# Performance work log

Measured on AMD Instinct MI355X. Metric: run time of the kernel, lower is better.

Reference implementation:

```python
import jax, jax.numpy as jnp
import numpy as np

NUM_HEADS = 12
EMBED_DIM = 768
HEAD_DIM = EMBED_DIM // NUM_HEADS


def _rope_cos_sin():
    # Faithful to source: RoPE is applied with seq_dim=1 on [b,h,n,d] tensors,
    # so the "position" axis is actually the HEAD axis (length NUM_HEADS).
    inv_freq = 1.0 / (10000.0 ** (jnp.arange(0, HEAD_DIM, 2, dtype=jnp.float32) / HEAD_DIM))
    t = jnp.arange(NUM_HEADS, dtype=jnp.float32)
    freqs = t[:, None] * inv_freq[None, :]            # [H, D/2]
    emb = jnp.concatenate([freqs, freqs], axis=-1)     # [H, D]
    cos = jnp.cos(emb)[None, :, None, :]               # [1, H, 1, D] broadcasts over seq
    sin = jnp.sin(emb)[None, :, None, :]
    return cos, sin


def _apply_rope(x, cos, sin):
    # x: [B, H, N, D]
    x1, x2 = jnp.split(x, 2, axis=-1)
    x_rot = jnp.concatenate([-x2, x1], axis=-1)
    return x * cos + x_rot * sin


def setup_inputs() -> dict:
    key = jax.random.key(0)
    k1, k2, k3, k4, k5 = jax.random.split(key, 5)
    B, N, E = 8, 1024, EMBED_DIM
    s_in = 1.0 / np.sqrt(E)
    return {
        "x": jax.random.normal(k1, (B, N, E), dtype=jnp.float32),
        "w_qkv": jax.random.uniform(k2, (E, 3 * E), dtype=jnp.float32, minval=-s_in, maxval=s_in),
        "b_qkv": jax.random.uniform(k3, (3 * E,), dtype=jnp.float32, minval=-s_in, maxval=s_in),
        "w_proj": jax.random.uniform(k4, (E, E), dtype=jnp.float32, minval=-s_in, maxval=s_in),
        "b_proj": jax.random.uniform(k5, (E,), dtype=jnp.float32, minval=-s_in, maxval=s_in),
    }


def reference(x, w_qkv, b_qkv, w_proj, b_proj):
    B, N, E = x.shape
    H, D = NUM_HEADS, HEAD_DIM
    scale = D ** (-0.5)

    qkv = x @ w_qkv + b_qkv                                  # [B, N, 3E]
    qkv = qkv.reshape(B, N, 3, H, D).transpose(2, 0, 3, 1, 4)  # [3, B, H, N, D]
    q, k, v = qkv[0], qkv[1], qkv[2]

    cos, sin = _rope_cos_sin()
    q = _apply_rope(q, cos, sin)
    k = _apply_rope(k, cos, sin)

    attn = jnp.einsum('bhid,bhjd->bhij', q, k) * scale       # [B, H, N, N]
    attn = jax.nn.softmax(attn, axis=-1)
    out = jnp.einsum('bhij,bhjd->bhid', attn, v)             # [B, H, N, D]
    out = out.transpose(0, 2, 1, 3).reshape(B, N, E)         # [B, N, E]
    return out @ w_proj + b_proj
```

## Files before the change

### kernel.cpp

```cpp
#include <hip/hip_runtime.h>
#include <math.h>

#define NH 12
#define HD 64
#define NSEQ 1024
#define BATCH 8
#define EMB 768
#define NQKV 2304
#define MROWS 8192

typedef _Float16 half8 __attribute__((ext_vector_type(8)));
typedef _Float16 half4 __attribute__((ext_vector_type(4)));
typedef _Float16 half2v __attribute__((ext_vector_type(2)));
typedef float f32x4 __attribute__((ext_vector_type(4)));
typedef float f32x16 __attribute__((ext_vector_type(16)));
typedef unsigned int u32;

#define MFMA16(a,b,c) __builtin_amdgcn_mfma_f32_16x16x32_f16(a, b, c, 0, 0, 0)
#define MFMA32(a,b,c) __builtin_amdgcn_mfma_f32_32x32x16_f16(a, b, c, 0, 0, 0)

#define QSCALE 0.18033688011112043f
#define EXPB 5.770780163555856f

#define ASYNC16(g, l)                                                          \
  __builtin_amdgcn_global_load_lds(                                            \
      (const __attribute__((address_space(1))) unsigned int*)(g),              \
      (__attribute__((address_space(3))) unsigned int*)(l), 16, 0, 0)

__device__ __forceinline__ void transpose_tile(const float* __restrict__ in,
                                               _Float16* __restrict__ out,
                                               int R, int C, int bx, int by,
                                               _Float16 (*T)[72]) {
  const int tr = by * 64, tc = bx * 64;
  const int r = threadIdx.x >> 2, s = threadIdx.x & 3;
  const float* src = in + (size_t)(tr + r) * C + tc + s * 16;
  _Float16* dst = &T[r][s * 16];
  #pragma unroll
  for (int i = 0; i < 4; ++i) {
    float4 v = ((const float4*)src)[i];
    dst[4*i+0] = (_Float16)v.x; dst[4*i+1] = (_Float16)v.y;
    dst[4*i+2] = (_Float16)v.z; dst[4*i+3] = (_Float16)v.w;
  }
  __syncthreads();
  alignas(16) _Float16 tmp[16];
  #pragma unroll
  for (int j = 0; j < 16; ++j) tmp[j] = T[s * 16 + j][r];
  half8* o = (half8*)(out + (size_t)(tc + r) * R + tr + s * 16);
  o[0] = *(half8*)&tmp[0];
  o[1] = *(half8*)&tmp[8];
}

__global__ __launch_bounds__(256) void prepass(const float* __restrict__ x,
                                               _Float16* __restrict__ xh,
                                               const float* __restrict__ wq,
                                               _Float16* __restrict__ wqT,
                                               const float* __restrict__ wp,
                                               _Float16* __restrict__ wpT) {
  __shared__ _Float16 T[64][72];
  const int bid = blockIdx.x;
  if (bid < 6144) {
    int i = bid * 256 + threadIdx.x;
    float4 v = ((const float4*)x)[i];
    half4 h = { (_Float16)v.x, (_Float16)v.y, (_Float16)v.z, (_Float16)v.w };
    ((half4*)xh)[i] = h;
  } else if (bid < 6576) {
    int idx = bid - 6144;
    transpose_tile(wq, wqT, EMB, NQKV, idx % 36, idx / 36, T);
  } else {
    int idx = bid - 6576;
    transpose_tile(wp, wpT, EMB, EMB, idx % 12, idx / 12, T);
  }
}

__device__ __forceinline__ int xcd_remap() {
  const int flat = blockIdx.y * gridDim.x + blockIdx.x;
  const int q = (gridDim.x * gridDim.y) >> 3;
  return (flat & 7) * q + (flat >> 3);
}

__global__ __launch_bounds__(256) void gemm_qkv(const _Float16* __restrict__ A,
                                                const _Float16* __restrict__ BT,
                                                const float* __restrict__ bias,
                                                _Float16* __restrict__ qo,
                                                _Float16* __restrict__ ko,
                                                _Float16* __restrict__ vo,
                                                int K) {
  const int BUFH = 128 * 32;
  __shared__ __align__(16) _Float16 As[2 * 128 * 32];
  __shared__ __align__(16) _Float16 Bs[2 * 128 * 32];
  const int tid = threadIdx.x;
  const int lane = tid & 63, wave = tid >> 6;
  const int quad = lane >> 4, l15 = lane & 15;
  const int wm = (wave >> 1) * 64, wn = (wave & 1) * 64;
  const int nf = xcd_remap();
  const int row0 = (nf / gridDim.x) * 128, col0 = (nf % gridDim.x) * 128;

  const int srow = lane >> 2;
  const int sseg = (lane & 3) ^ ((srow >> 1) & 3);
  const _Float16* gA = A + (size_t)(row0 + wave*32 + srow) * K + sseg * 8;
  const _Float16* gB = BT + (size_t)(col0 + wave*32 + srow) * K + sseg * 8;
  _Float16* lA = As + (wave * 32) * 32;
  _Float16* lB = Bs + (wave * 32) * 32;

  const int xq = (quad ^ ((l15 >> 1) & 3)) * 8;

  f32x4 acc[4][4];
  #pragma unroll
  for (int i = 0; i < 4; ++i)
    #pragma unroll
    for (int j = 0; j < 4; ++j) {
      f32x4 z = {0.f, 0.f, 0.f, 0.f};
      acc[i][j] = z;
    }

  ASYNC16(gA,          lA);
  ASYNC16(gA + 16 * K, lA + 16*32);
  ASYNC16(gB,          lB);
  ASYNC16(gB + 16 * K, lB + 16*32);
  __syncthreads();

  int buf = 0;
  for (int k0 = 0; k0 < K; k0 += 32) {
    if (k0 + 32 < K) {
      const int nb = (buf ^ 1) * BUFH;
      ASYNC16(gA + k0 + 32,          lA + nb);
      ASYNC16(gA + k0 + 32 + 16 * K, lA + nb + 16*32);
      ASYNC16(gB + k0 + 32,          lB + nb);
      ASYNC16(gB + k0 + 32 + 16 * K, lB + nb + 16*32);
    }
    const _Float16* Ab = As + buf * BUFH;
    const _Float16* Bb = Bs + buf * BUFH;
    half8 af[4], bf[4];
    #pragma unroll
    for (int mt = 0; mt < 4; ++mt)
      af[mt] = *(const half8*)(Ab + (wm + mt*16 + l15) * 32 + xq);
    #pragma unroll
    for (int nt = 0; nt < 4; ++nt)
      bf[nt] = *(const half8*)(Bb + (wn + nt*16 + l15) * 32 + xq);
    #pragma unroll
    for (int mt = 0; mt < 4; ++mt)
      #pragma unroll
      for (int nt = 0; nt < 4; ++nt)
        acc[mt][nt] = MFMA16(af[mt], bf[nt], acc[mt][nt]);
    __syncthreads();
    buf ^= 1;
  }

  float bcol[4];
  #pragma unroll
  for (int nt = 0; nt < 4; ++nt)
    bcol[nt] = bias[col0 + wn + nt*16 + l15];

  const int ch = col0 + wn;
  const int tt = ch / EMB;
  const int hh = (ch % EMB) >> 6;
  float cs[2], sn[2];
  if (tt < 2) {
    #pragma unroll
    for (int j = 0; j < 2; ++j) {
      float fi = (float)(j*16 + l15);
      float ang = (float)hh * expf(-0.28782313662425574f * fi);
      sincosf(ang, &sn[j], &cs[j]);
    }
  }
  #pragma unroll
  for (int mt = 0; mt < 4; ++mt) {
    int m0 = row0 + wm + mt*16 + quad*4;
    int b = m0 >> 10, n0 = m0 & 1023;
    size_t bh = (size_t)(b * NH + hh);
    if (tt == 2) {
      int np = (n0 & ~12) | ((n0 & 4) << 1) | ((n0 & 8) >> 1);
      #pragma unroll
      for (int nt = 0; nt < 4; ++nt) {
        int d = nt*16 + l15;
        half4 pk;
        #pragma unroll
        for (int r = 0; r < 4; ++r)
          pk[r] = (_Float16)(acc[mt][nt][r] + bcol[nt]);
        *(half4*)(vo + (bh * HD + d) * NSEQ + np) = pk;
      }
    } else {
      _Float16* dst = (tt == 0) ? qo : ko;
      const float sc = (tt == 0) ? QSCALE : 1.0f;
      #pragma unroll
      for (int j = 0; j < 2; ++j) {
        #pragma unroll
        for (int r = 0; r < 4; ++r) {
          float lo = acc[mt][j][r]     + bcol[j];
          float hi = acc[mt][j + 2][r] + bcol[j + 2];
          float nlo = (lo * cs[j] - hi * sn[j]) * sc;
          float nhi = (hi * cs[j] + lo * sn[j]) * sc;
          size_t rowoff = (bh * NSEQ + (size_t)(n0 + r)) * HD;
          dst[rowoff + j*16 + l15]      = (_Float16)nlo;
          dst[rowoff + j*16 + l15 + 32] = (_Float16)nhi;
        }
      }
    }
  }
}

__global__ __launch_bounds__(256) void gemm_proj(const _Float16* __restrict__ A,
                                                 const _Float16* __restrict__ BT,
                                                 const float* __restrict__ bias,
                                                 float* __restrict__ outf,
                                                 int K) {
  const int ABUF = 128 * 32, BBUF = 64 * 32;
  __shared__ __align__(16) _Float16 As[2 * ABUF];
  __shared__ __align__(16) _Float16 Bs[2 * BBUF];
  const int tid = threadIdx.x;
  const int lane = tid & 63, wave = tid >> 6;
  const int quad = lane >> 4, l15 = lane & 15;
  const int wm = (wave >> 1) * 64, wn = (wave & 1) * 32;
  const int nf = xcd_remap();
  const int row0 = (nf / gridDim.x) * 128, col0 = (nf % gridDim.x) * 64;

  const int srow = lane >> 2;
  const int sseg = (lane & 3) ^ ((srow >> 1) & 3);
  const _Float16* gA = A  + (size_t)(row0 + wave*32 + srow) * K + sseg * 8;
  const _Float16* gB = BT + (size_t)(col0 + wave*16 + srow) * K + sseg * 8;
  _Float16* lA = As + (wave * 32) * 32;
  _Float16* lB = Bs + (wave * 16) * 32;

  const int xq = (quad ^ ((l15 >> 1) & 3)) * 8;

  f32x4 acc[4][2];
  #pragma unroll
  for (int i = 0; i < 4; ++i)
    #pragma unroll
    for (int j = 0; j < 2; ++j) {
      f32x4 z = {0.f, 0.f, 0.f, 0.f};
      acc[i][j] = z;
    }

  ASYNC16(gA,          lA);
  ASYNC16(gA + 16 * K, lA + 16*32);
  ASYNC16(gB,          lB);
  __syncthreads();

  int buf = 0;
  for (int k0 = 0; k0 < K; k0 += 32) {
    if (k0 + 32 < K) {
      ASYNC16(gA + k0 + 32,          lA + (buf ^ 1) * ABUF);
      ASYNC16(gA + k0 + 32 + 16 * K, lA + (buf ^ 1) * ABUF + 16*32);
      ASYNC16(gB + k0 + 32,          lB + (buf ^ 1) * BBUF);
    }
    const _Float16* Ab = As + buf * ABUF;
    const _Float16* Bb = Bs + buf * BBUF;
    half8 af[4], bf[2];
    #pragma unroll
    for (int mt = 0; mt < 4; ++mt)
      af[mt] = *(const half8*)(Ab + (wm + mt*16 + l15) * 32 + xq);
    #pragma unroll
    for (int nt = 0; nt < 2; ++nt)
      bf[nt] = *(const half8*)(Bb + (wn + nt*16 + l15) * 32 + xq);
    #pragma unroll
    for (int mt = 0; mt < 4; ++mt)
      #pragma unroll
      for (int nt = 0; nt < 2; ++nt)
        acc[mt][nt] = MFMA16(af[mt], bf[nt], acc[mt][nt]);
    __syncthreads();
    buf ^= 1;
  }

  float bcol[2];
  #pragma unroll
  for (int nt = 0; nt < 2; ++nt)
    bcol[nt] = bias[col0 + wn + nt*16 + l15];
  #pragma unroll
  for (int mt = 0; mt < 4; ++mt) {
    int m0 = row0 + wm + mt*16 + quad*4;
    #pragma unroll
    for (int nt = 0; nt < 2; ++nt)
      #pragma unroll
      for (int r = 0; r < 4; ++r)
        outf[(size_t)(m0 + r) * EMB + col0 + wn + nt*16 + l15] =
            acc[mt][nt][r] + bcol[nt];
  }
}

__global__ __launch_bounds__(256) void attn_mfma32(const _Float16* __restrict__ q,
                                                   const _Float16* __restrict__ k,
                                                   const _Float16* __restrict__ vt,
                                                   _Float16* __restrict__ ao) {
  const int BUFH = 64 * 64;
  __shared__ __align__(16) _Float16 Ks[2 * 64 * 64];
  __shared__ __align__(16) _Float16 Vs[2 * 64 * 64];
  const int tid = threadIdx.x;
  const int lane = tid & 63, wave = tid >> 6;
  const int l31 = lane & 31, hi = lane >> 5;
  const int nf = xcd_remap();
  const int bh = nf >> 3;
  const int qrow = (nf & 7) * 128 + wave * 32 + l31;
  const size_t base = (size_t)bh * NSEQ * HD;

  const _Float16* qp = q + base + (size_t)qrow * HD + hi * 8;
  half8 qf[4];
  #pragma unroll
  for (int kh = 0; kh < 4; ++kh)
    qf[kh] = *(const half8*)(qp + kh * 16);

  const int srow8 = lane >> 3;
  const int sseg8 = lane & 7;
  const int wseg8 = sseg8 ^ (srow8 & 7);
  const _Float16* kg = k + base + (size_t)(wave*16 + srow8) * HD + wseg8 * 8;
  const _Float16* vg = vt + (size_t)bh * HD * NSEQ
                       + (size_t)(wave*16 + srow8) * NSEQ + wseg8 * 8;
  _Float16* uK = Ks + (wave * 16) * 64;
  _Float16* uV = Vs + (wave * 16) * 64;

  int xofs[4];
  #pragma unroll
  for (int kh = 0; kh < 4; ++kh)
    xofs[kh] = ((kh*2 + hi) ^ (l31 & 7)) * 8;

  f32x16 O[2];
  #pragma unroll
  for (int dt = 0; dt < 2; ++dt)
    #pragma unroll
    for (int r = 0; r < 16; ++r) O[dt][r] = 0.f;
  float l = 0.f;

  ASYNC16(kg,              uK);
  ASYNC16(kg + 8 * HD,     uK + 8*64);
  ASYNC16(vg,              uV);
  ASYNC16(vg + 8 * NSEQ,   uV + 8*64);
  __syncthreads();

  int buf = 0;
  for (int c0 = 0; c0 < NSEQ; c0 += 64) {
    if (c0 + 64 < NSEQ) {
      const int nb = (buf ^ 1) * BUFH;
      const _Float16* kc = kg + (size_t)(c0 + 64) * HD;
      ASYNC16(kc,                  uK + nb);
      ASYNC16(kc + 8 * HD,         uK + nb + 8*64);
      ASYNC16(vg + c0 + 64,        uV + nb);
      ASYNC16(vg + 8*NSEQ + c0 + 64, uV + nb + 8*64);
    }
    const _Float16* Kb = Ks + buf * BUFH;
    const _Float16* Vb = Vs + buf * BUFH;

    f32x16 ct[2];
    __builtin_amdgcn_s_setprio(1);
    #pragma unroll
    for (int kt = 0; kt < 2; ++kt) {
      #pragma unroll
      for (int r = 0; r < 16; ++r) ct[kt][r] = 0.f;
      #pragma unroll
      for (int kh = 0; kh < 4; ++kh) {
        half8 kf = *(const half8*)(Kb + (kt*32 + l31) * 64 + xofs[kh]);
        ct[kt] = MFMA32(kf, qf[kh], ct[kt]);
      }
    }
    __builtin_amdgcn_s_setprio(0);

    union { half2v v; int i; } ph2[16];
    float rs = 0.f;
    #pragma unroll
    for (int kt = 0; kt < 2; ++kt)
      #pragma unroll
      for (int rp = 0; rp < 8; ++rp) {
        float p0 = __builtin_amdgcn_exp2f(ct[kt][2*rp]     - EXPB);
        float p1 = __builtin_amdgcn_exp2f(ct[kt][2*rp + 1] - EXPB);
        rs += p0 + p1;
        half2v hp = { (_Float16)p0, (_Float16)p1 };
        ph2[kt*8 + rp].v = hp;
      }
    l += rs;

    __builtin_amdgcn_s_setprio(1);
    #pragma unroll
    for (int kh = 0; kh < 4; ++kh) {
      const int kt = kh >> 1;
      const int iA = kt*8 + (kh & 1)*4;
      union { half8 h; int d[4]; } pf;
      pf.d[0] = ph2[iA].i;     pf.d[1] = ph2[iA + 1].i;
      pf.d[2] = ph2[iA + 2].i; pf.d[3] = ph2[iA + 3].i;
      #pragma unroll
      for (int dt = 0; dt < 2; ++dt) {
        half8 vf = *(const half8*)(Vb + (dt*32 + l31) * 64 + xofs[kh]);
        O[dt] = MFMA32(vf, pf.h, O[dt]);
      }
    }
    __builtin_amdgcn_s_setprio(0);

    __syncthreads();
    buf ^= 1;
  }

  l += __shfl_xor(l, 32);

  const int b = bh / NH, hh = bh % NH;
  const float inv = 1.0f / l;
  _Float16* orow = ao + (size_t)(b * NSEQ + qrow) * EMB + hh * HD;
  #pragma unroll
  for (int dt = 0; dt < 2; ++dt)
    #pragma unroll
    for (int t = 0; t < 4; ++t) {
      int d0 = dt*32 + 8*t + 4*hi;
      half4 o4;
      #pragma unroll
      for (int j = 0; j < 4; ++j)
        o4[j] = (_Float16)(O[dt][4*t + j] * inv);
      *(half4*)(orow + d0) = o4;
    }
}

extern "C" void kernel_launch(void* const* d_in, const int* in_sizes, int n_in,
                              void* d_out, int out_size, void* d_ws, size_t ws_size,
                              hipStream_t stream) {
  const float* x      = (const float*)d_in[0];
  const float* w_qkv  = (const float*)d_in[1];
  const float* b_qkv  = (const float*)d_in[2];
  const float* w_proj = (const float*)d_in[3];
  const float* b_proj = (const float*)d_in[4];
  float* out = (float*)d_out;

  _Float16* xh  = (_Float16*)d_ws;
  _Float16* wqT = xh  + (size_t)MROWS * EMB;
  _Float16* wpT = wqT + (size_t)NQKV * EMB;
  _Float16* qh  = wpT + (size_t)EMB * EMB;
  _Float16* kh  = qh  + (size_t)BATCH*NH*NSEQ*HD;
  _Float16* vth = kh  + (size_t)BATCH*NH*NSEQ*HD;
  _Float16* aoh = vth + (size_t)BATCH*NH*NSEQ*HD;

  prepass<<<6720, 256, 0, stream>>>(x, xh, w_qkv, wqT, w_proj, wpT);

  gemm_qkv<<<dim3(NQKV/128, MROWS/128), 256, 0, stream>>>(
      xh, wqT, b_qkv, qh, kh, vth, EMB);

  attn_mfma32<<<dim3(NSEQ/128, BATCH*NH), 256, 0, stream>>>(qh, kh, vth, aoh);

  gemm_proj<<<dim3(EMB/64, MROWS/128), 256, 0, stream>>>(
      aoh, wpT, b_proj, out, EMB);
}
```

Before: 196.2 us.

## Make QKV GEMM persistent with next-tile prefetch overlapping epilogue; use packed cvt

The QKV projection GEMM now launches 768 blocks that each handle one or two 128x128 tiles: blocks with index below 384 take a second tile and start its first K-slice async loads before running the first tile's RoPE/bias epilogue, so load latency overlaps the stores. Launch bounds request 4 blocks per CU and the B fragment loads are interleaved with the MFMAs to lower register pressure. The attention kernel switches the fp32->fp16 probability conversion to the packed round-toward-zero cvt_pkrtz instruction, which changes rounding slightly. The uneven split (some blocks do two tiles, some one) can cause tail imbalance.

Measured after the change: 194.3 us. Within noise of the previous version (-1.0%).

```diff
diff --git a/kernel.cpp b/kernel.cpp
--- a/kernel.cpp
+++ b/kernel.cpp
@@ -12,6 +12,7 @@
 typedef _Float16 half8 __attribute__((ext_vector_type(8)));
 typedef _Float16 half4 __attribute__((ext_vector_type(4)));
 typedef _Float16 half2v __attribute__((ext_vector_type(2)));
+typedef __fp16 fp16x2 __attribute__((ext_vector_type(2)));
 typedef float f32x4 __attribute__((ext_vector_type(4)));
 typedef float f32x16 __attribute__((ext_vector_type(16)));
 typedef unsigned int u32;
@@ -78,124 +79,142 @@
   return (flat & 7) * q + (flat >> 3);
 }
 
-__global__ __launch_bounds__(256) void gemm_qkv(const _Float16* __restrict__ A,
-                                                const _Float16* __restrict__ BT,
-                                                const float* __restrict__ bias,
-                                                _Float16* __restrict__ qo,
-                                                _Float16* __restrict__ ko,
-                                                _Float16* __restrict__ vo,
-                                                int K) {
+__global__ __launch_bounds__(256, 4) void gemm_qkv(const _Float16* __restrict__ A,
+                                                   const _Float16* __restrict__ BT,
+                                                   const float* __restrict__ bias,
+                                                   _Float16* __restrict__ qo,
+                                                   _Float16* __restrict__ ko,
+                                                   _Float16* __restrict__ vo,
+                                                   int K) {
   const int BUFH = 128 * 32;
-  __shared__ __align__(16) _Float16 As[2 * 128 * 32];
-  __shared__ __align__(16) _Float16 Bs[2 * 128 * 32];
+  __shared__ __align__(16) _Float16 As[2 * BUFH];
+  __shared__ __align__(16) _Float16 Bs[2 * BUFH];
   const int tid = threadIdx.x;
   const int lane = tid & 63, wave = tid >> 6;
   const int quad = lane >> 4, l15 = lane & 15;
   const int wm = (wave >> 1) * 64, wn = (wave & 1) * 64;
-  const int nf = xcd_remap();
-  const int row0 = (nf / gridDim.x) * 128, col0 = (nf % gridDim.x) * 128;
 
   const int srow = lane >> 2;
   const int sseg = (lane & 3) ^ ((srow >> 1) & 3);
+  _Float16* lA = As + (wave * 32) * 32;
+  _Float16* lB = Bs + (wave * 32) * 32;
+  const int xq = (quad ^ ((l15 >> 1) & 3)) * 8;
+
+  int f = blockIdx.x;
+  int nf = (f & 7) * 144 + (f >> 3);
+  int row0 = (nf / 18) * 128, col0 = (nf % 18) * 128;
   const _Float16* gA = A + (size_t)(row0 + wave*32 + srow) * K + sseg * 8;
   const _Float16* gB = BT + (size_t)(col0 + wave*32 + srow) * K + sseg * 8;
-  _Float16* lA = As + (wave * 32) * 32;
-  _Float16* lB = Bs + (wave * 32) * 32;
-
-  const int xq = (quad ^ ((l15 >> 1) & 3)) * 8;
-
-  f32x4 acc[4][4];
-  #pragma unroll
-  for (int i = 0; i < 4; ++i)
-    #pragma unroll
-    for (int j = 0; j < 4; ++j) {
-      f32x4 z = {0.f, 0.f, 0.f, 0.f};
-      acc[i][j] = z;
-    }
 
   ASYNC16(gA,          lA);
   ASYNC16(gA + 16 * K, lA + 16*32);
   ASYNC16(gB,          lB);
   ASYNC16(gB + 16 * K, lB + 16*32);
-  __syncthreads();
-
-  int buf = 0;
-  for (int k0 = 0; k0 < K; k0 += 32) {
-    if (k0 + 32 < K) {
-      const int nb = (buf ^ 1) * BUFH;
-      ASYNC16(gA + k0 + 32,          lA + nb);
-      ASYNC16(gA + k0 + 32 + 16 * K, lA + nb + 16*32);
-      ASYNC16(gB + k0 + 32,          lB + nb);
-      ASYNC16(gB + k0 + 32 + 16 * K, lB + nb + 16*32);
-    }
-    const _Float16* Ab = As + buf * BUFH;
-    const _Float16* Bb = Bs + buf * BUFH;
-    half8 af[4], bf[4];
-    #pragma unroll
-    for (int mt = 0; mt < 4; ++mt)
-      af[mt] = *(const half8*)(Ab + (wm + mt*16 + l15) * 32 + xq);
+
+  while (true) {
+    f32x4 acc[4][4];
+    #pragma unroll
+    for (int i = 0; i < 4; ++i)
+      #pragma unroll
+      for (int j = 0; j < 4; ++j) {
+        f32x4 z = {0.f, 0.f, 0.f, 0.f};
+        acc[i][j] = z;
+      }
+    __syncthreads();
+
+    int buf = 0;
+    for (int k0 = 0; k0 < K; k0 += 32) {
+      if (k0 + 32 < K) {
+        const int nb = (buf ^ 1) * BUFH;
+        ASYNC16(gA + k0 + 32,          lA + nb);
+        ASYNC16(gA + k0 + 32 + 16 * K, lA + nb + 16*32);
+        ASYNC16(gB + k0 + 32,          lB + nb);
+        ASYNC16(gB + k0 + 32 + 16 * K, lB + nb + 16*32);
+      }
+      const _Float16* Ab = As + buf * BUFH;
+      const _Float16* Bb = Bs + buf * BUFH;
+      half8 af[4];
+      #pragma unroll
+      for (int mt = 0; mt < 4; ++mt)
+        af[mt] = *(const half8*)(Ab + (wm + mt*16 + l15) * 32 + xq);
+      #pragma unroll
+      for (int nt = 0; nt < 4; ++nt) {
+        half8 bf = *(const half8*)(Bb + (wn + nt*16 + l15) * 32 + xq);
+        #pragma unroll
+        for (int mt = 0; mt < 4; ++mt)
+          acc[mt][nt] = MFMA16(af[mt], bf, acc[mt][nt]);
+      }
+      __syncthreads();
+      buf ^= 1;
+    }
+
+    const int erow = row0, ecol = col0;
+    const bool more = (f < 384);
+    if (more) {
+      f += 768;
+      nf = (f & 7) * 144 + (f >> 3);
+      row0 = (nf / 18) * 128;
+      col0 = (nf % 18) * 128;
+      gA = A + (size_t)(row0 + wave*32 + srow) * K + sseg * 8;
+      gB = BT + (size_t)(col0 + wave*32 + srow) * K + sseg * 8;
+      ASYNC16(gA,          lA);
+      ASYNC16(gA + 16 * K, lA + 16*32);
+      ASYNC16(gB,          lB);
+      ASYNC16(gB + 16 * K, lB + 16*32);
+    }
+
+    float bcol[4];
     #pragma unroll
     for (int nt = 0; nt < 4; ++nt)
-      bf[nt] = *(const half8*)(Bb + (wn + nt*16 + l15) * 32 + xq);
-    #pragma unroll
-    for (int mt = 0; mt < 4; ++mt)
-      #pragma unroll
-      for (int nt = 0; nt < 4; ++nt)
-        acc[mt][nt] = MFMA16(af[mt], bf[nt], acc[mt][nt]);
-    __syncthreads();
-    buf ^= 1;
-  }
-
-  float bcol[4];
-  #pragma unroll
-  for (int nt = 0; nt < 4; ++nt)
-    bcol[nt] = bias[col0 + wn + nt*16 + l15];
-
-  const int ch = col0 + wn;
-  const int tt = ch / EMB;
-  const int hh = (ch % EMB) >> 6;
-  float cs[2], sn[2];
-  if (tt < 2) {
-    #pragma unroll
-    for (int j = 0; j < 2; ++j) {
-      float fi = (float)(j*16 + l15);
-      float ang = (float)hh * expf(-0.28782313662425574f * fi);
-      sincosf(ang, &sn[j], &cs[j]);
-    }
-  }
-  #pragma unroll
-  for (int mt = 0; mt < 4; ++mt) {
-    int m0 = row0 + wm + mt*16 + quad*4;
-    int b = m0 >> 10, n0 = m0 & 1023;
-    size_t bh = (size_t)(b * NH + hh);
-    if (tt == 2) {
-      int np = (n0 & ~12) | ((n0 & 4) << 1) | ((n0 & 8) >> 1);
-      #pragma unroll
-      for (int nt = 0; nt < 4; ++nt) {
-        int d = nt*16 + l15;
-        half4 pk;
+      bcol[nt] = bias[ecol + wn + nt*16 + l15];
+
+    const int ch = ecol + wn;
+    const int tt = ch / EMB;
+    const int hh = (ch % EMB) >> 6;
+    float cs[2], sn[2];
+    if (tt < 2) {
+      #pragma unroll
+      for (int j = 0; j < 2; ++j) {
+        float fi = (float)(j*16 + l15);
+        float ang = (float)hh * expf(-0.28782313662425574f * fi);
+        sincosf(ang, &sn[j], &cs[j]);
+      }
+    }
+    #pragma unroll
+    for (int mt = 0; mt < 4; ++mt) {
+      int m0 = erow + wm + mt*16 + quad*4;
+      int b = m0 >> 10, n0 = m0 & 1023;
+      size_t bh = (size_t)(b * NH + hh);
+      if (tt == 2) {
+        int np = (n0 & ~12) | ((n0 & 4) << 1) | ((n0 & 8) >> 1);
         #pragma unroll
-        for (int r = 0; r < 4; ++r)
-          pk[r] = (_Float16)(acc[mt][nt][r] + bcol[nt]);
-        *(half4*)(vo + (bh * HD + d) * NSEQ + np) = pk;
-      }
-    } else {
-      _Float16* dst = (tt == 0) ? qo : ko;
-      const float sc = (tt == 0) ? QSCALE : 1.0f;
-      #pragma unroll
-      for (int j = 0; j < 2; ++j) {
+        for (int nt = 0; nt < 4; ++nt) {
+          int d = nt*16 + l15;
+          half4 pk;
+          #pragma unroll
+          for (int r = 0; r < 4; ++r)
+            pk[r] = (_Float16)(acc[mt][nt][r] + bcol[nt]);
+          *(half4*)(vo + (bh * HD + d) * NSEQ + np) = pk;
+        }
+      } else {
+        _Float16* dst = (tt == 0) ? qo : ko;
+        const float sc = (tt == 0) ? QSCALE : 1.0f;
         #pragma unroll
-        for (int r = 0; r < 4; ++r) {
-          float lo = acc[mt][j][r]     + bcol[j];
-          float hi = acc[mt][j + 2][r] + bcol[j + 2];
-          float nlo = (lo * cs[j] - hi * sn[j]) * sc;
-          float nhi = (hi * cs[j] + lo * sn[j]) * sc;
-          size_t rowoff = (bh * NSEQ + (size_t)(n0 + r)) * HD;
-          dst[rowoff + j*16 + l15]      = (_Float16)nlo;
-          dst[rowoff + j*16 + l15 + 32] = (_Float16)nhi;
+        for (int j = 0; j < 2; ++j) {
+          #pragma unroll
+          for (int r = 0; r < 4; ++r) {
+            float lo = acc[mt][j][r]     + bcol[j];
+            float hi = acc[mt][j + 2][r] + bcol[j + 2];
+            float nlo = (lo * cs[j] - hi * sn[j]) * sc;
+            float nhi = (hi * cs[j] + lo * sn[j]) * sc;
+            size_t rowoff = (bh * NSEQ + (size_t)(n0 + r)) * HD;
+            dst[rowoff + j*16 + l15]      = (_Float16)nlo;
+            dst[rowoff + j*16 + l15 + 32] = (_Float16)nhi;
+          }
         }
       }
     }
+    if (!more) break;
   }
 }
 
@@ -353,7 +372,7 @@
     }
     __builtin_amdgcn_s_setprio(0);
 
-    union { half2v v; int i; } ph2[16];
+    union { half2v v; fp16x2 f; int i; } ph2[16];
     float rs = 0.f;
     #pragma unroll
     for (int kt = 0; kt < 2; ++kt)
@@ -362,8 +381,7 @@
         float p0 = __builtin_amdgcn_exp2f(ct[kt][2*rp]     - EXPB);
         float p1 = __builtin_amdgcn_exp2f(ct[kt][2*rp + 1] - EXPB);
         rs += p0 + p1;
-        half2v hp = { (_Float16)p0, (_Float16)p1 };
-        ph2[kt*8 + rp].v = hp;
+        ph2[kt*8 + rp].f = __builtin_amdgcn_cvt_pkrtz(p0, p1);
       }
     l += rs;
 
@@ -425,8 +443,7 @@
 
   prepass<<<6720, 256, 0, stream>>>(x, xh, w_qkv, wqT, w_proj, wpT);
 
-  gemm_qkv<<<dim3(NQKV/128, MROWS/128), 256, 0, stream>>>(
-      xh, wqT, b_qkv, qh, kh, vth, EMB);
+  gemm_qkv<<<768, 256, 0, stream>>>(xh, wqT, b_qkv, qh, kh, vth, EMB);
 
   attn_mfma32<<<dim3(NSEQ/128, BATCH*NH), 256, 0, stream>>>(qh, kh, vth, aoh);
 
```
